# Kernel optimization log

Hardware: AMD Instinct MI355X
Metric: run time of the kernel (lower is better)

The kernel has to match this reference:

```python
import jax, jax.numpy as jnp
import numpy as np

B, K, H, W = 16, 64, 160, 160
EPS = 1e-5


def setup_inputs() -> dict:
    key = jax.random.key(0)
    k1, k2 = jax.random.split(key)
    # keypoints[..., 0] = x in [0, W-1], keypoints[..., 1] = y in [0, H-1]
    kp = jax.random.uniform(k1, (B, K, 2), dtype=jnp.float32)
    keypoints = kp * jnp.array([W - 1.0, H - 1.0], dtype=jnp.float32)
    DetectionMap = jax.random.uniform(k2, (B, K, H, W), dtype=jnp.float32)
    return {
        "keypoints": keypoints,
        "reconDetectionMap_std_x": jnp.float32(6.0),
        "reconDetectionMap_std_y": jnp.float32(6.0),
        "correlation": jnp.float32(0.1),
        "DetectionMap": DetectionMap,
    }


def reference(keypoints, reconDetectionMap_std_x, reconDetectionMap_std_y, correlation, DetectionMap):
    sx = reconDetectionMap_std_x
    sy = reconDetectionMap_std_y
    rho = correlation
    Bv, Kv, Hv, Wv = DetectionMap.shape

    one_m_rho2 = 1.0 - rho * rho
    den = 1.0 / (2.0 * jnp.pi * sx * sy * jnp.sqrt(one_m_rho2))
    num1 = -1.0 / (2.0 * one_m_rho2)

    ii = jnp.arange(Hv, dtype=keypoints.dtype)  # rows (y)
    jj = jnp.arange(Wv, dtype=keypoints.dtype)  # cols (x)
    # dy: [B,K,H,1], dx: [B,K,1,W] -> broadcast to [B,K,H,W] only inside num2
    dy = ii[None, None, :, None] - keypoints[:, :, 1][:, :, None, None]
    dx = jj[None, None, None, :] - keypoints[:, :, 0][:, :, None, None]

    num2 = (dy * dy) / (sy * sy) + (dx * dx) / (sx * sx) \
        - (2.0 * rho / (sx * sy)) * dy * dx  # [B,K,H,W]
    scoreMap = den * jnp.exp(num1 * num2)  # [B,K,H,W]

    denom = jnp.sum(scoreMap, axis=1, keepdims=True) + EPS  # [B,1,H,W]
    return scoreMap / denom
```

## Files before the change

kernel.cpp:

```cpp
#include <hip/hip_runtime.h>

#define KK 64
#define HH 160
#define WW 160
#define HWPIX (HH * WW)
#define EPSF 1e-5f

__global__ __launch_bounds__(64) void recon_confmap_kernel(
    const float* __restrict__ kp,
    const float* __restrict__ sx_p,
    const float* __restrict__ sy_p,
    const float* __restrict__ rho_p,
    float* __restrict__ out)
{
    __shared__ float2 skp[KK];

    const int b   = blockIdx.y;
    const int tid = threadIdx.x;

    skp[tid] = ((const float2*)(kp + (size_t)b * KK * 2))[tid];

    const float sx  = sx_p[0];
    const float sy  = sy_p[0];
    const float rho = rho_p[0];
    __syncthreads();

    const float L2E   = 1.44269504088896340736f;
    const float omr2  = 1.0f - rho * rho;
    const float num1  = -0.5f / omr2;
    const float ca    = num1 / (sy * sy) * L2E;
    const float cb    = num1 / (sx * sx) * L2E;
    const float cc    = num1 * (-2.0f * rho / (sx * sy)) * L2E;
    const float c2b   = 2.0f * cb;
    const float epsod = EPSF * (2.0f * 3.14159265358979323846f * sx * sy * sqrtf(omr2));

    const int P  = (blockIdx.x * 64 + tid) * 4;
    const int i  = P / WW;
    const int j0 = P - i * WW;
    const float fi = (float)i;
    const float fj = (float)j0;

    float s0 = 0.f, s1 = 0.f, s2 = 0.f, s3 = 0.f;
#pragma unroll
    for (int k = 0; k < KK; ++k) {
        const float dy  = fi - skp[k].y;
        const float dx  = fj - skp[k].x;
        const float tA  = cc * dy;
        const float tyy = ca * dy * dy;
        const float a0  = fmaf(tA, dx, fmaf(cb * dx, dx, tyy));
        float d = fmaf(c2b, dx, tA) + cb;
        const float a1 = a0 + d; d += c2b;
        const float a2 = a1 + d; d += c2b;
        const float a3 = a2 + d;
        s0 += __builtin_amdgcn_exp2f(a0);
        s1 += __builtin_amdgcn_exp2f(a1);
        s2 += __builtin_amdgcn_exp2f(a2);
        s3 += __builtin_amdgcn_exp2f(a3);
    }

    const float i0 = 1.0f / (s0 + epsod);
    const float i1 = 1.0f / (s1 + epsod);
    const float i2 = 1.0f / (s2 + epsod);
    const float i3 = 1.0f / (s3 + epsod);

    float fi2 = fi, fj2 = fj;
    asm("" : "+v"(fi2), "+v"(fj2));

    float* op = out + (size_t)b * KK * HWPIX + P;

#pragma unroll
    for (int k = 0; k < KK; ++k) {
        const float dy  = fi2 - skp[k].y;
        const float dx  = fj2 - skp[k].x;
        const float tA  = cc * dy;
        const float tyy = ca * dy * dy;
        const float a0  = fmaf(tA, dx, fmaf(cb * dx, dx, tyy));
        float d = fmaf(c2b, dx, tA) + cb;
        const float a1 = a0 + d; d += c2b;
        const float a2 = a1 + d; d += c2b;
        const float a3 = a2 + d;
        float4 v;
        v.x = __builtin_amdgcn_exp2f(a0) * i0;
        v.y = __builtin_amdgcn_exp2f(a1) * i1;
        v.z = __builtin_amdgcn_exp2f(a2) * i2;
        v.w = __builtin_amdgcn_exp2f(a3) * i3;
        *(float4*)(op + (size_t)k * HWPIX) = v;
    }
}

extern "C" void kernel_launch(void* const* d_in, const int* in_sizes, int n_in,
                              void* d_out, int out_size, void* d_ws, size_t ws_size,
                              hipStream_t stream) {
    const float* kp    = (const float*)d_in[0];
    const float* sx_p  = (const float*)d_in[1];
    const float* sy_p  = (const float*)d_in[2];
    const float* rho_p = (const float*)d_in[3];
    float* out = (float*)d_out;

    const int B = in_sizes[0] / (KK * 2);
    dim3 grid(HWPIX / (64 * 4), B);
    recon_confmap_kernel<<<grid, 64, 0, stream>>>(kp, sx_p, sy_p, rho_p, out);
}
```

Before: 174.7 us.

## Split keypoint loop across four waves with shared-memory sum reduction

Each block now has 256 threads. Four wavefronts each handle 16 of the 64 keypoints for the same 256 pixels, so a block still covers one pixel tile. The partial denominators are combined through shared memory and a barrier, and each wave writes its own 16 output channels. The aim is more waves in flight per pixel tile and a shorter serial exp chain per thread, which helps hide the store traffic. The cost is a shared-memory reduction and a block-wide sync.

```diff
diff --git a/kernel.cpp b/kernel.cpp
--- a/kernel.cpp
+++ b/kernel.cpp
@@ -6,7 +6,7 @@
 #define HWPIX (HH * WW)
 #define EPSF 1e-5f
 
-__global__ __launch_bounds__(64) void recon_confmap_kernel(
+__global__ __launch_bounds__(256) void recon_confmap_kernel(
     const float* __restrict__ kp,
     const float* __restrict__ sx_p,
     const float* __restrict__ sy_p,
@@ -14,11 +14,16 @@
     float* __restrict__ out)
 {
     __shared__ float2 skp[KK];
+    __shared__ float4 red[4][64];
 
-    const int b   = blockIdx.y;
-    const int tid = threadIdx.x;
+    const int b = blockIdx.y;
+    const int t = threadIdx.x;
+    const int q = t >> 6;
+    const int g = t & 63;
 
-    skp[tid] = ((const float2*)(kp + (size_t)b * KK * 2))[tid];
+    if (t < KK) {
+        skp[t] = ((const float2*)(kp + (size_t)b * KK * 2))[t];
+    }
 
     const float sx  = sx_p[0];
     const float sy  = sy_p[0];
@@ -34,20 +39,22 @@
     const float c2b   = 2.0f * cb;
     const float epsod = EPSF * (2.0f * 3.14159265358979323846f * sx * sy * sqrtf(omr2));
 
-    const int P  = (blockIdx.x * 64 + tid) * 4;
+    const int P  = blockIdx.x * 256 + g * 4;
     const int i  = P / WW;
     const int j0 = P - i * WW;
     const float fi = (float)i;
     const float fj = (float)j0;
 
+    const int k0 = q * 16;
+
     float s0 = 0.f, s1 = 0.f, s2 = 0.f, s3 = 0.f;
 #pragma unroll
-    for (int k = 0; k < KK; ++k) {
-        const float dy  = fi - skp[k].y;
-        const float dx  = fj - skp[k].x;
+    for (int kk = 0; kk < 16; ++kk) {
+        const float2 K2 = skp[k0 + kk];
+        const float dy  = fi - K2.y;
+        const float dx  = fj - K2.x;
         const float tA  = cc * dy;
-        const float tyy = ca * dy * dy;
-        const float a0  = fmaf(tA, dx, fmaf(cb * dx, dx, tyy));
+        const float a0  = fmaf(tA, dx, fmaf(cb * dx, dx, ca * dy * dy));
         float d = fmaf(c2b, dx, tA) + cb;
         const float a1 = a0 + d; d += c2b;
         const float a2 = a1 + d; d += c2b;
@@ -58,23 +65,30 @@
         s3 += __builtin_amdgcn_exp2f(a3);
     }
 
-    const float i0 = 1.0f / (s0 + epsod);
-    const float i1 = 1.0f / (s1 + epsod);
-    const float i2 = 1.0f / (s2 + epsod);
-    const float i3 = 1.0f / (s3 + epsod);
+    red[q][g] = make_float4(s0, s1, s2, s3);
+    __syncthreads();
+
+    const float4 r0 = red[0][g];
+    const float4 r1 = red[1][g];
+    const float4 r2 = red[2][g];
+    const float4 r3 = red[3][g];
+    const float i0 = 1.0f / (r0.x + r1.x + r2.x + r3.x + epsod);
+    const float i1 = 1.0f / (r0.y + r1.y + r2.y + r3.y + epsod);
+    const float i2 = 1.0f / (r0.z + r1.z + r2.z + r3.z + epsod);
+    const float i3 = 1.0f / (r0.w + r1.w + r2.w + r3.w + epsod);
 
     float fi2 = fi, fj2 = fj;
     asm("" : "+v"(fi2), "+v"(fj2));
 
-    float* op = out + (size_t)b * KK * HWPIX + P;
+    float* op = out + (size_t)b * KK * HWPIX + (size_t)k0 * HWPIX + P;
 
 #pragma unroll
-    for (int k = 0; k < KK; ++k) {
-        const float dy  = fi2 - skp[k].y;
-        const float dx  = fj2 - skp[k].x;
+    for (int kk = 0; kk < 16; ++kk) {
+        const float2 K2 = skp[k0 + kk];
+        const float dy  = fi2 - K2.y;
+        const float dx  = fj2 - K2.x;
         const float tA  = cc * dy;
-        const float tyy = ca * dy * dy;
-        const float a0  = fmaf(tA, dx, fmaf(cb * dx, dx, tyy));
+        const float a0  = fmaf(tA, dx, fmaf(cb * dx, dx, ca * dy * dy));
         float d = fmaf(c2b, dx, tA) + cb;
         const float a1 = a0 + d; d += c2b;
         const float a2 = a1 + d; d += c2b;
@@ -84,7 +98,7 @@
         v.y = __builtin_amdgcn_exp2f(a1) * i1;
         v.z = __builtin_amdgcn_exp2f(a2) * i2;
         v.w = __builtin_amdgcn_exp2f(a3) * i3;
-        *(float4*)(op + (size_t)k * HWPIX) = v;
+        *(float4*)(op + (size_t)kk * HWPIX) = v;
     }
 }
 
@@ -98,6 +112,6 @@
     float* out = (float*)d_out;
 
     const int B = in_sizes[0] / (KK * 2);
-    dim3 grid(HWPIX / (64 * 4), B);
-    recon_confmap_kernel<<<grid, 64, 0, stream>>>(kp, sx_p, sy_p, rho_p, out);
+    dim3 grid(HWPIX / 256, B);
+    recon_confmap_kernel<<<grid, 256, 0, stream>>>(kp, sx_p, sy_p, rho_p, out);
 }
```

After: 168.2 us. 3.7% less time.
